# Optimization experiments

Hardware: AMD Instinct MI355X
Metric: run time of the kernel (lower is better)

## Reference

```python
import jax, jax.numpy as jnp
import numpy as np

E = 1024      # embed_dim
H = 16        # num_heads
D = E // H    # head_dim
T = 2048      # tgt_len
S = 2048      # src_len
B = 8         # batch
SCALE = D ** -0.5
EPS = 1e-6


def setup_inputs() -> dict:
    key = jax.random.key(0)
    ks = jax.random.split(key, 8)
    w = lambda k: jax.random.normal(k, (E, E), jnp.float32) * (1.0 / np.sqrt(E))
    return {
        "query": jax.random.normal(ks[0], (T, B, E), jnp.float32),
        "key_in": jax.random.normal(ks[1], (S, B, E), jnp.float32),
        "value": jax.random.normal(ks[2], (S, B, E), jnp.float32),
        "wq": w(ks[3]), "bq": jnp.zeros((E,), jnp.float32),
        "wk": w(ks[4]), "bk": jnp.zeros((E,), jnp.float32),
        "wv": w(ks[5]), "bv": jnp.zeros((E,), jnp.float32),
        "wo": w(ks[6]), "bo": jnp.zeros((E,), jnp.float32),
    }


def _to_heads(x):
    # (L, B, E) -> (B*H, L, D), matching fairseq's view/transpose
    L = x.shape[0]
    return x.reshape(L, B * H, D).transpose(1, 0, 2)


def reference(query, key_in, value, wq, bq, wk, bk, wv, bv, wo, bo):
    # projections (fairseq scales q by head_dim**-0.5)
    q = (query @ wq.T + bq) * SCALE
    k = key_in @ wk.T + bk
    v = value @ wv.T + bv
    # cosFormer feature map: ReLU then cos/sin positional reweighting
    q = jax.nn.relu(_to_heads(q))   # (BH, T, D)
    k = jax.nn.relu(_to_heads(k))   # (BH, S, D)
    v = _to_heads(v)                # (BH, S, D)
    # sin(pi/2 * i / len), cos(pi/2 * i / len) for i in 1..len
    iq = jnp.arange(1, T + 1, dtype=jnp.float32) / T
    ik = jnp.arange(1, S + 1, dtype=jnp.float32) / S
    half_pi = jnp.float32(np.pi / 2)
    sq = jnp.sin(half_pi * iq)[None, :, None]
    cq = jnp.cos(half_pi * iq)[None, :, None]
    sk = jnp.sin(half_pi * ik)[None, :, None]
    ck = jnp.cos(half_pi * ik)[None, :, None]
    q2 = jnp.concatenate([q * sq, q * cq], axis=-1)   # (BH, T, 2D)
    k2 = jnp.concatenate([k * sk, k * ck], axis=-1)   # (BH, S, 2D)
    # linear attention: O(S*D^2) instead of O(S^2*D)
    kv = jnp.einsum('bsd,bse->bde', k2, v)            # (BH, 2D, D)
    num = jnp.einsum('btd,bde->bte', q2, kv)          # (BH, T, D)
    den = jnp.einsum('btd,bd->bt', q2, k2.sum(axis=1))
    out = num / jnp.maximum(den, EPS)[..., None]
    out = out.transpose(1, 0, 2).reshape(T, B, E)     # back to (T, B, E)
    return out @ wo.T + bo
```

## Files before the change

### kernel.cpp

```cpp
#include <hip/hip_runtime.h>
#include <hip/hip_bf16.h>

using bf16 = __hip_bfloat16;
typedef __attribute__((ext_vector_type(8))) short short8;
typedef __attribute__((ext_vector_type(4))) float f32x4;

#define GLL16(gp, lp) __builtin_amdgcn_global_load_lds( \
    (__attribute__((address_space(1))) void*)(gp),      \
    (__attribute__((address_space(3))) void*)(lp), 16, 0, 0)

__device__ __forceinline__ bf16 f2b(float x) { return __float2bfloat16(x); }
__device__ __forceinline__ float s2f(short x) {
  unsigned u = ((unsigned)(unsigned short)x) << 16;
  return __uint_as_float(u);
}
__device__ __forceinline__ short f2s(float x) {
  bf16 h = __float2bfloat16(x);
  return *reinterpret_cast<short*>(&h);
}

#define TRIG_C (1.5707963268f / 2048.0f)

__global__ void cvt_f32_bf16(const float* __restrict__ src, bf16* __restrict__ dst, int n8)
{
  const int i = blockIdx.x * 256 + threadIdx.x;
  if (i >= n8) return;
  const f32x4 a = ((const f32x4*)src)[i * 2];
  const f32x4 b = ((const f32x4*)src)[i * 2 + 1];
  short8 o;
#pragma unroll
  for (int j = 0; j < 4; ++j) { o[j] = f2s(a[j]); o[4 + j] = f2s(b[j]); }
  *(short8*)&dst[i * 8] = o;
}

template<int MODE>
__global__ __launch_bounds__(512, 2)
void proj_gemm(const bf16* __restrict__ A, const bf16* __restrict__ W,
               const float* __restrict__ bias, void* __restrict__ O)
{
  constexpr int K = 1024;
  constexpr int BK = 64;
  extern __shared__ __align__(16) char smem[];
  bf16* lds = (bf16*)smem;

  const int tid = threadIdx.x;
  const int w = tid >> 6, l = tid & 63;
  const int quad = l >> 4, l16 = l & 15;
  const int lrow = l >> 3;
  const int scol = ((l & 7) ^ lrow) << 3;
  const int wm = w >> 2, wn = w & 3;

  const int bid = blockIdx.x;
  const int xcd = bid & 7, idx = bid >> 3;
  const int ni = idx & 3;
  const int mi = xcd + 8 * (idx >> 2);
  const long mblk = (long)mi * 256;
  const int  nblk = ni * 256;

  const bf16* Ag = A + mblk * K;
  const bf16* Wg = W + (long)nblk * K;

  f32x4 acc[8][4] = {};

  auto STAGE = [&](int buf, int kt) {
    bf16* As = lds + buf * 32768;
    bf16* Bs = As + 16384;
#pragma unroll
    for (int i = 0; i < 4; ++i) {
      const int c = w * 4 + i;
      const int r = c * 8 + lrow;
      GLL16(Ag + (long)r * K + kt + scol, &As[c * 512]);
      GLL16(Wg + (long)r * K + kt + scol, &Bs[c * 512]);
    }
  };

  STAGE(0, 0);
  __syncthreads();

  for (int t = 0; t < K / BK; ++t) {
    if (t + 1 < K / BK) STAGE((t + 1) & 1, (t + 1) * BK);
    const bf16* As = lds + (t & 1) * 32768;
    const bf16* Bs = As + 16384;
#pragma unroll
    for (int kk = 0; kk < BK; kk += 32) {
      const int ko8 = (kk + quad * 8) >> 3;
      short8 a[8], b[4];
#pragma unroll
      for (int sb = 0; sb < 8; ++sb) {
        const int row = wm * 128 + sb * 16 + l16;
        a[sb] = *(const short8*)&As[row * 64 + ((ko8 ^ (row & 7)) << 3)];
      }
#pragma unroll
      for (int u = 0; u < 4; ++u) {
        const int row = wn * 64 + u * 16 + l16;
        b[u] = *(const short8*)&Bs[row * 64 + ((ko8 ^ (row & 7)) << 3)];
      }
#pragma unroll
      for (int sb = 0; sb < 8; ++sb)
#pragma unroll
        for (int u = 0; u < 4; ++u)
          acc[sb][u] = __builtin_amdgcn_mfma_f32_16x16x32_bf16(a[sb], b[u], acc[sb][u], 0, 0, 0);
    }
    __syncthreads();
  }

  if (MODE == 3) {
#pragma unroll
    for (int sb = 0; sb < 8; ++sb) {
      const int row0 = (int)mblk + wm * 128 + sb * 16 + quad * 4;
#pragma unroll
      for (int u = 0; u < 4; ++u) {
        const int col = nblk + wn * 64 + u * 16 + l16;
        const float bc = bias[col];
#pragma unroll
        for (int j = 0; j < 4; ++j)
          ((float*)O)[(long)(row0 + j) * 1024 + col] = acc[sb][u][j] + bc;
      }
    }
  } else {
    bf16* T = lds;
#pragma unroll
    for (int sb = 0; sb < 8; ++sb) {
#pragma unroll
      for (int u = 0; u < 4; ++u) {
        const int lc = wn * 64 + u * 16 + l16;
        const int h = lc >> 6, d = lc & 63;
        const float bc = bias[nblk + lc];
#pragma unroll
        for (int j = 0; j < 4; ++j) {
          const int lr = wm * 128 + sb * 16 + quad * 4 + j;
          float v = acc[sb][u][j] + bc;
          if (MODE == 0) v = fmaxf(v * 0.125f, 0.f);
          if (MODE == 1) v = fmaxf(v, 0.f);
          int ix;
          if (MODE == 0) {
            const int tt = lr >> 3, bb = lr & 7;
            const int dc = (d >> 3) ^ (tt & 7);
            ix = (((bb * 4 + h) * 32 + tt) * 8 + dc) * 8 + (d & 7);
          } else {
            const int ss = lr >> 3, bb = lr & 7;
            const int sc = (ss >> 3) ^ (d & 3);
            ix = (((bb * 4 + h) * 64 + d) * 4 + sc) * 8 + (ss & 7);
          }
          T[ix] = f2b(v);
        }
      }
    }
    __syncthreads();
    const int hbase = nblk >> 6;
    const int sbase = (int)(mblk >> 3);
#pragma unroll
    for (int i = 0; i < 16; ++i) {
      const int c = i * 512 + tid;
      if (MODE == 0) {
        const int dch = c & 7, tt = (c >> 3) & 31, h = (c >> 8) & 3, bb = c >> 10;
        const short8 val = *(const short8*)&T[(((bb * 4 + h) * 32 + tt) * 8 + (dch ^ (tt & 7))) * 8];
        bf16* dst = (bf16*)O + ((long)(bb * 16 + hbase + h) * 2048 + sbase + tt) * 64 + dch * 8;
        *(short8*)dst = val;
      } else {
        const int sc = c & 3, d = (c >> 2) & 63, h = (c >> 8) & 3, bb = c >> 10;
        const short8 val = *(const short8*)&T[(((bb * 4 + h) * 64 + d) * 4 + (sc ^ (d & 3))) * 8];
        bf16* dst = (bf16*)O + ((long)(bb * 16 + hbase + h) * 64 + d) * 2048 + sbase + sc * 8;
        *(short8*)dst = val;
      }
    }
  }
}

__global__ void ksum2_kernel(const bf16* __restrict__ KhT, float* __restrict__ ksum2)
{
  const int gw = (blockIdx.x * 256 + threadIdx.x) >> 6;
  const int l = threadIdx.x & 63;
  const int bh = gw >> 6, d = gw & 63;
  const bf16* row = KhT + ((long)bh * 64 + d) * 2048;
  float ss = 0.f, cc = 0.f;
#pragma unroll
  for (int i = 0; i < 4; ++i) {
    short8 v = *(const short8*)&row[i * 512 + l * 8];
#pragma unroll
    for (int j = 0; j < 8; ++j) {
      const int s = i * 512 + l * 8 + j;
      const float ang = (float)(s + 1) * TRIG_C;
      const float f = s2f(v[j]);
      ss += f * __sinf(ang);
      cc += f * __cosf(ang);
    }
  }
#pragma unroll
  for (int off = 32; off > 0; off >>= 1) {
    ss += __shfl_down(ss, off);
    cc += __shfl_down(cc, off);
  }
  if (l == 0) {
    ksum2[bh * 128 + d]      = ss;
    ksum2[bh * 128 + 64 + d] = cc;
  }
}

__global__ void kv_gemm(const bf16* __restrict__ VhT, const bf16* __restrict__ KhT,
                        bf16* __restrict__ kv2)
{
  __shared__ __align__(16) bf16 As[64 * 64];
  __shared__ __align__(16) bf16 Bs[64 * 64];
  const int bh = blockIdx.x;
  const int fl = blockIdx.y;
  const int tid = threadIdx.x, w = tid >> 6, l = tid & 63;
  const int quad = l >> 4, l16 = l & 15;
  const int lrow = l >> 3, lcol = (l & 7) * 8;
  const bf16* Vg = VhT + (long)bh * 64 * 2048;
  const bf16* Kg = KhT + (long)bh * 64 * 2048;
  const int ar = tid >> 2, ac = (tid & 3) * 16;

  f32x4 acc[4] = {};

  for (int kt = 0; kt < 2048; kt += 64) {
#pragma unroll
    for (int i = 0; i < 2; ++i) {
      const int c = w * 2 + i, r = c * 8 + lrow;
      GLL16(Kg + (long)r * 2048 + kt + lcol, &Bs[c * 512]);
    }
    short8 v0 = *(const short8*)&Vg[(long)ar * 2048 + kt + ac];
    short8 v1 = *(const short8*)&Vg[(long)ar * 2048 + kt + ac + 8];
    short8 o0, o1;
#pragma unroll
    for (int j = 0; j < 8; ++j) {
      const int sA = kt + ac + j, sB = sA + 8;
      const float angA = (float)(sA + 1) * TRIG_C, angB = (float)(sB + 1) * TRIG_C;
      const float wA = fl ? __cosf(angA) : __sinf(angA);
      const float wB = fl ? __cosf(angB) : __sinf(angB);
      o0[j] = f2s(s2f(v0[j]) * wA);
      o1[j] = f2s(s2f(v1[j]) * wB);
    }
    *(short8*)&As[ar * 64 + ac]     = o0;
    *(short8*)&As[ar * 64 + ac + 8] = o1;
    __syncthreads();
#pragma unroll
    for (int kk = 0; kk < 64; kk += 32) {
      const int ko = kk + quad * 8;
      short8 a = *(const short8*)&As[(w * 16 + l16) * 64 + ko];
      short8 b[4];
#pragma unroll
      for (int u = 0; u < 4; ++u) b[u] = *(const short8*)&Bs[(u * 16 + l16) * 64 + ko];
#pragma unroll
      for (int tn = 0; tn < 4; ++tn)
        acc[tn] = __builtin_amdgcn_mfma_f32_16x16x32_bf16(a, b[tn], acc[tn], 0, 0, 0);
    }
    __syncthreads();
  }
  bf16* out = kv2 + (long)bh * 128 * 64 + fl * 64 * 64;
#pragma unroll
  for (int tn = 0; tn < 4; ++tn) {
    const int d = tn * 16 + l16;
#pragma unroll
    for (int j = 0; j < 4; ++j) {
      const int e = w * 16 + quad * 4 + j;
      out[e * 64 + d] = f2b(acc[tn][j]);
    }
  }
}

__global__ void den_kernel(const bf16* __restrict__ Qh, const float* __restrict__ ksum2,
                           float* __restrict__ dinv)
{
  __shared__ float ks[128];
  const int bh = blockIdx.y;
  const int t = blockIdx.x * 256 + threadIdx.x;
  if (threadIdx.x < 128) ks[threadIdx.x] = ksum2[bh * 128 + threadIdx.x];
  __syncthreads();
  const bf16* q = Qh + ((long)bh * 2048 + t) * 64;
  float d1 = 0.f, d2 = 0.f;
#pragma unroll
  for (int i = 0; i < 8; ++i) {
    short8 v = *(const short8*)&q[i * 8];
#pragma unroll
    for (int j = 0; j < 8; ++j) {
      const float f = s2f(v[j]);
      d1 += f * ks[i * 8 + j];
      d2 += f * ks[64 + i * 8 + j];
    }
  }
  const float ang = (float)(t + 1) * TRIG_C;
  const float den = __sinf(ang) * d1 + __cosf(ang) * d2;
  dinv[bh * 2048 + t] = 1.f / fmaxf(den, 1e-6f);
}

__global__ void attn_out(const bf16* __restrict__ Qh, const bf16* __restrict__ kv2,
                         const float* __restrict__ dinv, bf16* __restrict__ att)
{
  __shared__ __align__(16) bf16 Qs[128 * 64];
  __shared__ __align__(16) bf16 Ks[128 * 64];
  const int bh = blockIdx.y;
  const int t0 = blockIdx.x * 128;
  const int tid = threadIdx.x, w = tid >> 6, l = tid & 63;
  const int quad = l >> 4, l16 = l & 15;
  const int lrow = l >> 3, lcol = (l & 7) * 8;
  const bf16* Qg = Qh + ((long)bh * 2048 + t0) * 64;
  const bf16* Kg = kv2 + (long)bh * 128 * 64;
#pragma unroll
  for (int i = 0; i < 4; ++i) {
    const int c = w * 4 + i, r = c * 8 + lrow;
    GLL16(Qg + (long)r * 64 + lcol, &Qs[c * 512]);
  }
#pragma unroll
  for (int i = 0; i < 4; ++i) {
    const int c = w * 4 + i, r = c * 8 + lrow;
    GLL16(Kg + (long)r * 64 + lcol, &Ks[c * 512]);
  }
  __syncthreads();

  f32x4 accs[2][4] = {}, accc[2][4] = {};
#pragma unroll
  for (int kk = 0; kk < 64; kk += 32) {
    const int ko = kk + quad * 8;
    short8 a[2], bs[4], bc[4];
#pragma unroll
    for (int u = 0; u < 2; ++u) a[u] = *(const short8*)&Qs[(w * 32 + u * 16 + l16) * 64 + ko];
#pragma unroll
    for (int u = 0; u < 4; ++u) {
      bs[u] = *(const short8*)&Ks[(u * 16 + l16) * 64 + ko];
      bc[u] = *(const short8*)&Ks[(64 + u * 16 + l16) * 64 + ko];
    }
#pragma unroll
    for (int tm = 0; tm < 2; ++tm)
#pragma unroll
      for (int tn = 0; tn < 4; ++tn) {
        accs[tm][tn] = __builtin_amdgcn_mfma_f32_16x16x32_bf16(a[tm], bs[tn], accs[tm][tn], 0, 0, 0);
        accc[tm][tn] = __builtin_amdgcn_mfma_f32_16x16x32_bf16(a[tm], bc[tn], accc[tm][tn], 0, 0, 0);
      }
  }
  const int bb = bh >> 4, h = bh & 15;
#pragma unroll
  for (int tm = 0; tm < 2; ++tm)
#pragma unroll
    for (int j = 0; j < 4; ++j) {
      const int tr = w * 32 + tm * 16 + quad * 4 + j;
      const int t = t0 + tr;
      const float di = dinv[bh * 2048 + t];
      const float ang = (float)(t + 1) * TRIG_C;
      const float sn = __sinf(ang), cs = __cosf(ang);
#pragma unroll
      for (int tn = 0; tn < 4; ++tn) {
        const int e = tn * 16 + l16;
        const float v = (sn * accs[tm][tn][j] + cs * accc[tm][tn][j]) * di;
        att[((long)t * 8 + bb) * 1024 + h * 64 + e] = f2b(v);
      }
    }
}

extern "C" void kernel_launch(void* const* d_in, const int* in_sizes, int n_in,
                              void* d_out, int out_size, void* d_ws, size_t ws_size,
                              hipStream_t stream)
{
  const float* query  = (const float*)d_in[0];
  const float* key_in = (const float*)d_in[1];
  const float* value  = (const float*)d_in[2];
  const float* wq = (const float*)d_in[3];  const float* bq = (const float*)d_in[4];
  const float* wk = (const float*)d_in[5];  const float* bk = (const float*)d_in[6];
  const float* wv = (const float*)d_in[7];  const float* bv = (const float*)d_in[8];
  const float* wo = (const float*)d_in[9];  const float* bo = (const float*)d_in[10];

  char* ws = (char*)d_ws;
  float* ksum2 = (float*)(ws);
  float* dinv  = (float*)(ws + 65536);
  bf16*  kv2   = (bf16*)(ws + 1114112);
  bf16*  Wslot = (bf16*)(ws + 3211264);
  bf16*  R1    = (bf16*)(ws + 5308416);
  bf16*  KhT = R1, *ATT = R1;
  bf16*  D1 = (bf16*)d_out;
  bf16*  D2 = (bf16*)d_out + 16777216;

  const int PROJ_LDS = 131072;
  hipFuncSetAttribute((const void*)&proj_gemm<0>, hipFuncAttributeMaxDynamicSharedMemorySize, PROJ_LDS);
  hipFuncSetAttribute((const void*)&proj_gemm<1>, hipFuncAttributeMaxDynamicSharedMemorySize, PROJ_LDS);
  hipFuncSetAttribute((const void*)&proj_gemm<2>, hipFuncAttributeMaxDynamicSharedMemorySize, PROJ_LDS);
  hipFuncSetAttribute((const void*)&proj_gemm<3>, hipFuncAttributeMaxDynamicSharedMemorySize, PROJ_LDS);

  dim3 blk(256);
  dim3 pblk(512);
  dim3 gproj(256);
  const int nBig = 16777216 / 8, gBig = nBig / 256;
  const int nW   = 1048576 / 8,  gW   = nW / 256;

  hipLaunchKernelGGL(cvt_f32_bf16, dim3(gBig), blk, 0, stream, key_in, D1, nBig);
  hipLaunchKernelGGL(cvt_f32_bf16, dim3(gW),   blk, 0, stream, wk, Wslot, nW);
  hipLaunchKernelGGL((proj_gemm<1>), gproj, pblk, PROJ_LDS, stream, D1, Wslot, bk, KhT);
  hipLaunchKernelGGL(ksum2_kernel, dim3(2048), blk, 0, stream, KhT, ksum2);
  hipLaunchKernelGGL(cvt_f32_bf16, dim3(gBig), blk, 0, stream, value, D2, nBig);
  hipLaunchKernelGGL(cvt_f32_bf16, dim3(gW),   blk, 0, stream, wv, Wslot, nW);
  hipLaunchKernelGGL((proj_gemm<2>), gproj, pblk, PROJ_LDS, stream, D2, Wslot, bv, D1);
  hipLaunchKernelGGL(kv_gemm, dim3(128, 2), blk, 0, stream, D1, KhT, kv2);
  hipLaunchKernelGGL(cvt_f32_bf16, dim3(gBig), blk, 0, stream, query, D2, nBig);
  hipLaunchKernelGGL(cvt_f32_bf16, dim3(gW),   blk, 0, stream, wq, Wslot, nW);
  hipLaunchKernelGGL((proj_gemm<0>), gproj, pblk, PROJ_LDS, stream, D2, Wslot, bq, D1);
  hipLaunchKernelGGL(den_kernel, dim3(8, 128), blk, 0, stream, D1, ksum2, dinv);
  hipLaunchKernelGGL(attn_out, dim3(16, 128), blk, 0, stream, D1, kv2, dinv, ATT);
  hipLaunchKernelGGL(cvt_f32_bf16, dim3(gW),   blk, 0, stream, wo, Wslot, nW);
  hipLaunchKernelGGL((proj_gemm<3>), gproj, pblk, PROJ_LDS, stream, ATT, Wslot, bo, d_out);
}
```

Before: 451.6 us.

## Fuse ksum and denominator kernels into kv_gemm and attn_out with pipelining

Measured after the change: 439.1 us. 2.8% less time.

```diff
diff --git a/kernel.cpp b/kernel.cpp
--- a/kernel.cpp
+++ b/kernel.cpp
@@ -56,7 +56,6 @@
   const int mi = xcd + 8 * (idx >> 2);
   const long mblk = (long)mi * 256;
   const int  nblk = ni * 256;
-
   const bf16* Ag = A + mblk * K;
   const bf16* Wg = W + (long)nblk * K;
 
@@ -167,86 +166,76 @@
   }
 }
 
-__global__ void ksum2_kernel(const bf16* __restrict__ KhT, float* __restrict__ ksum2)
-{
-  const int gw = (blockIdx.x * 256 + threadIdx.x) >> 6;
-  const int l = threadIdx.x & 63;
-  const int bh = gw >> 6, d = gw & 63;
-  const bf16* row = KhT + ((long)bh * 64 + d) * 2048;
-  float ss = 0.f, cc = 0.f;
-#pragma unroll
-  for (int i = 0; i < 4; ++i) {
-    short8 v = *(const short8*)&row[i * 512 + l * 8];
-#pragma unroll
-    for (int j = 0; j < 8; ++j) {
-      const int s = i * 512 + l * 8 + j;
-      const float ang = (float)(s + 1) * TRIG_C;
-      const float f = s2f(v[j]);
-      ss += f * __sinf(ang);
-      cc += f * __cosf(ang);
-    }
-  }
-#pragma unroll
-  for (int off = 32; off > 0; off >>= 1) {
-    ss += __shfl_down(ss, off);
-    cc += __shfl_down(cc, off);
-  }
-  if (l == 0) {
-    ksum2[bh * 128 + d]      = ss;
-    ksum2[bh * 128 + 64 + d] = cc;
-  }
-}
-
 __global__ void kv_gemm(const bf16* __restrict__ VhT, const bf16* __restrict__ KhT,
-                        bf16* __restrict__ kv2)
-{
-  __shared__ __align__(16) bf16 As[64 * 64];
-  __shared__ __align__(16) bf16 Bs[64 * 64];
+                        bf16* __restrict__ kv2, float* __restrict__ ksum2)
+{
+  __shared__ __align__(16) bf16 Vs[2][64 * 64];
+  __shared__ __align__(16) bf16 Ks[2][64 * 64];
   const int bh = blockIdx.x;
   const int fl = blockIdx.y;
   const int tid = threadIdx.x, w = tid >> 6, l = tid & 63;
   const int quad = l >> 4, l16 = l & 15;
-  const int lrow = l >> 3, lcol = (l & 7) * 8;
+  const int lrow = l >> 3;
+  const int scol = ((l & 7) ^ lrow) << 3;
   const bf16* Vg = VhT + (long)bh * 64 * 2048;
   const bf16* Kg = KhT + (long)bh * 64 * 2048;
-  const int ar = tid >> 2, ac = (tid & 3) * 16;
+  const int ar = tid >> 2, ac8 = (tid & 3) * 2;
+  const int r7 = ar & 7;
 
   f32x4 acc[4] = {};
-
-  for (int kt = 0; kt < 2048; kt += 64) {
+  float ps = 0.f;
+
+  auto VSTAGE = [&](int buf, int kt) {
 #pragma unroll
     for (int i = 0; i < 2; ++i) {
       const int c = w * 2 + i, r = c * 8 + lrow;
-      GLL16(Kg + (long)r * 2048 + kt + lcol, &Bs[c * 512]);
-    }
-    short8 v0 = *(const short8*)&Vg[(long)ar * 2048 + kt + ac];
-    short8 v1 = *(const short8*)&Vg[(long)ar * 2048 + kt + ac + 8];
+      GLL16(Vg + (long)r * 2048 + kt + scol, &Vs[buf][c * 512]);
+    }
+  };
+  auto KLOAD = [&](int kt, short8& ka, short8& kb) {
+    ka = *(const short8*)&Kg[(long)ar * 2048 + kt + ac8 * 8];
+    kb = *(const short8*)&Kg[(long)ar * 2048 + kt + ac8 * 8 + 8];
+  };
+  auto KSCALE = [&](int buf, int kt, short8 ka, short8 kb) {
     short8 o0, o1;
 #pragma unroll
     for (int j = 0; j < 8; ++j) {
-      const int sA = kt + ac + j, sB = sA + 8;
+      const int sA = kt + ac8 * 8 + j, sB = sA + 8;
       const float angA = (float)(sA + 1) * TRIG_C, angB = (float)(sB + 1) * TRIG_C;
       const float wA = fl ? __cosf(angA) : __sinf(angA);
       const float wB = fl ? __cosf(angB) : __sinf(angB);
-      o0[j] = f2s(s2f(v0[j]) * wA);
-      o1[j] = f2s(s2f(v1[j]) * wB);
-    }
-    *(short8*)&As[ar * 64 + ac]     = o0;
-    *(short8*)&As[ar * 64 + ac + 8] = o1;
-    __syncthreads();
+      const float fA = s2f(ka[j]), fB = s2f(kb[j]);
+      o0[j] = f2s(fA * wA);  o1[j] = f2s(fB * wB);
+      ps += fA * wA + fB * wB;
+    }
+    *(short8*)&Ks[buf][ar * 64 + ((ac8 ^ r7) << 3)]       = o0;
+    *(short8*)&Ks[buf][ar * 64 + (((ac8 + 1) ^ r7) << 3)] = o1;
+  };
+
+  { short8 ka, kb; KLOAD(0, ka, kb); VSTAGE(0, 0); KSCALE(0, 0, ka, kb); }
+  __syncthreads();
+
+  for (int t = 0; t < 32; ++t) {
+    short8 ka, kb;
+    if (t < 31) { KLOAD((t + 1) * 64, ka, kb); VSTAGE((t + 1) & 1, (t + 1) * 64); }
+    const int buf = t & 1;
 #pragma unroll
     for (int kk = 0; kk < 64; kk += 32) {
-      const int ko = kk + quad * 8;
-      short8 a = *(const short8*)&As[(w * 16 + l16) * 64 + ko];
+      const int ko8 = (kk + quad * 8) >> 3;
+      const int rowa = w * 16 + l16;
+      short8 a = *(const short8*)&Vs[buf][rowa * 64 + ((ko8 ^ (l16 & 7)) << 3)];
       short8 b[4];
 #pragma unroll
-      for (int u = 0; u < 4; ++u) b[u] = *(const short8*)&Bs[(u * 16 + l16) * 64 + ko];
+      for (int u = 0; u < 4; ++u)
+        b[u] = *(const short8*)&Ks[buf][(u * 16 + l16) * 64 + ((ko8 ^ (l16 & 7)) << 3)];
 #pragma unroll
       for (int tn = 0; tn < 4; ++tn)
         acc[tn] = __builtin_amdgcn_mfma_f32_16x16x32_bf16(a, b[tn], acc[tn], 0, 0, 0);
     }
+    if (t < 31) KSCALE((t + 1) & 1, (t + 1) * 64, ka, kb);
     __syncthreads();
   }
+
   bf16* out = kv2 + (long)bh * 128 * 64 + fl * 64 * 64;
 #pragma unroll
   for (int tn = 0; tn < 4; ++tn) {
@@ -257,68 +246,77 @@
       out[e * 64 + d] = f2b(acc[tn][j]);
     }
   }
-}
-
-__global__ void den_kernel(const bf16* __restrict__ Qh, const float* __restrict__ ksum2,
-                           float* __restrict__ dinv)
-{
-  __shared__ float ks[128];
-  const int bh = blockIdx.y;
-  const int t = blockIdx.x * 256 + threadIdx.x;
-  if (threadIdx.x < 128) ks[threadIdx.x] = ksum2[bh * 128 + threadIdx.x];
-  __syncthreads();
-  const bf16* q = Qh + ((long)bh * 2048 + t) * 64;
-  float d1 = 0.f, d2 = 0.f;
-#pragma unroll
-  for (int i = 0; i < 8; ++i) {
-    short8 v = *(const short8*)&q[i * 8];
-#pragma unroll
-    for (int j = 0; j < 8; ++j) {
-      const float f = s2f(v[j]);
-      d1 += f * ks[i * 8 + j];
-      d2 += f * ks[64 + i * 8 + j];
-    }
-  }
-  const float ang = (float)(t + 1) * TRIG_C;
-  const float den = __sinf(ang) * d1 + __cosf(ang) * d2;
-  dinv[bh * 2048 + t] = 1.f / fmaxf(den, 1e-6f);
+  ps += __shfl_xor(ps, 1);
+  ps += __shfl_xor(ps, 2);
+  if ((tid & 3) == 0) ksum2[bh * 128 + fl * 64 + ar] = ps;
 }
 
 __global__ void attn_out(const bf16* __restrict__ Qh, const bf16* __restrict__ kv2,
-                         const float* __restrict__ dinv, bf16* __restrict__ att)
+                         const float* __restrict__ ksum2g, bf16* __restrict__ att)
 {
   __shared__ __align__(16) bf16 Qs[128 * 64];
   __shared__ __align__(16) bf16 Ks[128 * 64];
+  __shared__ float ks[128];
+  __shared__ float dinv_s[128];
   const int bh = blockIdx.y;
   const int t0 = blockIdx.x * 128;
   const int tid = threadIdx.x, w = tid >> 6, l = tid & 63;
   const int quad = l >> 4, l16 = l & 15;
-  const int lrow = l >> 3, lcol = (l & 7) * 8;
+  const int lrow = l >> 3;
+  const int scol = ((l & 7) ^ lrow) << 3;
   const bf16* Qg = Qh + ((long)bh * 2048 + t0) * 64;
   const bf16* Kg = kv2 + (long)bh * 128 * 64;
 #pragma unroll
   for (int i = 0; i < 4; ++i) {
     const int c = w * 4 + i, r = c * 8 + lrow;
-    GLL16(Qg + (long)r * 64 + lcol, &Qs[c * 512]);
+    GLL16(Qg + (long)r * 64 + scol, &Qs[c * 512]);
   }
 #pragma unroll
   for (int i = 0; i < 4; ++i) {
     const int c = w * 4 + i, r = c * 8 + lrow;
-    GLL16(Kg + (long)r * 64 + lcol, &Ks[c * 512]);
-  }
+    GLL16(Kg + (long)r * 64 + scol, &Ks[c * 512]);
+  }
+  if (tid < 128) ks[tid] = ksum2g[bh * 128 + tid];
   __syncthreads();
 
+  {
+    const int r = tid >> 1, half = tid & 1;
+    float d1 = 0.f, d2 = 0.f;
+#pragma unroll
+    for (int blk = 0; blk < 4; ++blk) {
+      const int g = (half * 4 + blk) ^ (r & 7);
+      const short8 v = *(const short8*)&Qs[r * 64 + g * 8];
+#pragma unroll
+      for (int j = 0; j < 8; ++j) {
+        const float f = s2f(v[j]);
+        const int d = half * 32 + blk * 8 + j;
+        d1 += f * ks[d];
+        d2 += f * ks[64 + d];
+      }
+    }
+    d1 += __shfl_xor(d1, 1);
+    d2 += __shfl_xor(d2, 1);
+    if (half == 0) {
+      const float ang = (float)(t0 + r + 1) * TRIG_C;
+      const float den = __sinf(ang) * d1 + __cosf(ang) * d2;
+      dinv_s[r] = 1.f / fmaxf(den, 1e-6f);
+    }
+  }
+
   f32x4 accs[2][4] = {}, accc[2][4] = {};
 #pragma unroll
   for (int kk = 0; kk < 64; kk += 32) {
-    const int ko = kk + quad * 8;
+    const int ko8 = (kk + quad * 8) >> 3;
     short8 a[2], bs[4], bc[4];
 #pragma unroll
-    for (int u = 0; u < 2; ++u) a[u] = *(const short8*)&Qs[(w * 32 + u * 16 + l16) * 64 + ko];
+    for (int u = 0; u < 2; ++u) {
+      const int row = w * 32 + u * 16 + l16;
+      a[u] = *(const short8*)&Qs[row * 64 + ((ko8 ^ (row & 7)) << 3)];
+    }
 #pragma unroll
     for (int u = 0; u < 4; ++u) {
-      bs[u] = *(const short8*)&Ks[(u * 16 + l16) * 64 + ko];
-      bc[u] = *(const short8*)&Ks[(64 + u * 16 + l16) * 64 + ko];
+      bs[u] = *(const short8*)&Ks[(u * 16 + l16) * 64 + ((ko8 ^ (l16 & 7)) << 3)];
+      bc[u] = *(const short8*)&Ks[(64 + u * 16 + l16) * 64 + ((ko8 ^ (l16 & 7)) << 3)];
     }
 #pragma unroll
     for (int tm = 0; tm < 2; ++tm)
@@ -328,6 +326,8 @@
         accc[tm][tn] = __builtin_amdgcn_mfma_f32_16x16x32_bf16(a[tm], bc[tn], accc[tm][tn], 0, 0, 0);
       }
   }
+  __syncthreads();
+
   const int bb = bh >> 4, h = bh & 15;
 #pragma unroll
   for (int tm = 0; tm < 2; ++tm)
@@ -335,7 +335,7 @@
     for (int j = 0; j < 4; ++j) {
       const int tr = w * 32 + tm * 16 + quad * 4 + j;
       const int t = t0 + tr;
-      const float di = dinv[bh * 2048 + t];
+      const float di = dinv_s[tr];
       const float ang = (float)(t + 1) * TRIG_C;
       const float sn = __sinf(ang), cs = __cosf(ang);
 #pragma unroll
@@ -361,7 +361,6 @@
 
   char* ws = (char*)d_ws;
   float* ksum2 = (float*)(ws);
-  float* dinv  = (float*)(ws + 65536);
   bf16*  kv2   = (bf16*)(ws + 1114112);
   bf16*  Wslot = (bf16*)(ws + 3211264);
   bf16*  R1    = (bf16*)(ws + 5308416);
@@ -384,16 +383,14 @@
   hipLaunchKernelGGL(cvt_f32_bf16, dim3(gBig), blk, 0, stream, key_in, D1, nBig);
   hipLaunchKernelGGL(cvt_f32_bf16, dim3(gW),   blk, 0, stream, wk, Wslot, nW);
   hipLaunchKernelGGL((proj_gemm<1>), gproj, pblk, PROJ_LDS, stream, D1, Wslot, bk, KhT);
-  hipLaunchKernelGGL(ksum2_kernel, dim3(2048), blk, 0, stream, KhT, ksum2);
   hipLaunchKernelGGL(cvt_f32_bf16, dim3(gBig), blk, 0, stream, value, D2, nBig);
   hipLaunchKernelGGL(cvt_f32_bf16, dim3(gW),   blk, 0, stream, wv, Wslot, nW);
   hipLaunchKernelGGL((proj_gemm<2>), gproj, pblk, PROJ_LDS, stream, D2, Wslot, bv, D1);
-  hipLaunchKernelGGL(kv_gemm, dim3(128, 2), blk, 0, stream, D1, KhT, kv2);
+  hipLaunchKernelGGL(kv_gemm, dim3(128, 2), blk, 0, stream, D1, KhT, kv2, ksum2);
   hipLaunchKernelGGL(cvt_f32_bf16, dim3(gBig), blk, 0, stream, query, D2, nBig);
   hipLaunchKernelGGL(cvt_f32_bf16, dim3(gW),   blk, 0, stream, wq, Wslot, nW);
   hipLaunchKernelGGL((proj_gemm<0>), gproj, pblk, PROJ_LDS, stream, D2, Wslot, bq, D1);
-  hipLaunchKernelGGL(den_kernel, dim3(8, 128), blk, 0, stream, D1, ksum2, dinv);
-  hipLaunchKernelGGL(attn_out, dim3(16, 128), blk, 0, stream, D1, kv2, dinv, ATT);
+  hipLaunchKernelGGL(attn_out, dim3(16, 128), blk, 0, stream, D1, kv2, ksum2, ATT);
   hipLaunchKernelGGL(cvt_f32_bf16, dim3(gW),   blk, 0, stream, wo, Wslot, nW);
   hipLaunchKernelGGL((proj_gemm<3>), gproj, pblk, PROJ_LDS, stream, ATT, Wslot, bo, d_out);
 }
```
